# Kernel tuning notes

Hardware: AMD Instinct MI355X
Metric: run time of the kernel (lower is better)

The kernel has to match this reference:

```python
import jax, jax.numpy as jnp
import numpy as np

BN_EPS = 1e-5
W_BITS = 2
A_BITS = 2


def _quantize_k(x, k):
    # uniform quantization of x in [0,1] to k bits, straight-through estimator
    n = float(2 ** k - 1)
    q = jnp.round(x * n) / n
    return x + jax.lax.stop_gradient(q - x)


def _quant_weight(w, k):
    # DoReFa-style weight quantization to [-1, 1]
    t = jnp.tanh(w)
    t = t / (2.0 * jnp.max(jnp.abs(t))) + 0.5
    return 2.0 * _quantize_k(t, k) - 1.0


def _quant_act(x, k):
    # DoReFa-style activation quantization: clamp to [0,1], quantize
    return _quantize_k(jnp.clip(x, 0.0, 1.0), k)


def _conv3x3(x, w, stride=1):
    # x: [N,C,H,W], w: [O,I,3,3], padding=1
    return jax.lax.conv_general_dilated(
        x, w, window_strides=(stride, stride), padding=((1, 1), (1, 1)),
        dimension_numbers=('NCHW', 'OIHW', 'NCHW'))


def _bn(x, gamma, beta, mean, var):
    inv = gamma / jnp.sqrt(var + BN_EPS)           # [C]
    return x * inv[None, :, None, None] + (beta - mean * inv)[None, :, None, None]


def setup_inputs() -> dict:
    key = jax.random.key(0)
    ks = jax.random.split(key, 8)
    N, C, H, W = 64, 256, 28, 28
    x = jax.random.normal(ks[0], (N, C, H, W), dtype=jnp.float32)
    w1 = jax.random.normal(ks[1], (C, C, 3, 3), dtype=jnp.float32) * 0.05
    w2 = jax.random.normal(ks[2], (C, C, 3, 3), dtype=jnp.float32) * 0.05
    g1 = jnp.ones((C,), jnp.float32)
    b1 = jnp.zeros((C,), jnp.float32)
    m1 = jax.random.normal(ks[3], (C,), dtype=jnp.float32) * 0.1
    v1 = jax.random.uniform(ks[4], (C,), dtype=jnp.float32) + 0.5
    g2 = jnp.ones((C,), jnp.float32)
    b2 = jnp.zeros((C,), jnp.float32)
    m2 = jax.random.normal(ks[5], (C,), dtype=jnp.float32) * 0.1
    v2 = jax.random.uniform(ks[6], (C,), dtype=jnp.float32) + 0.5
    return {'x': x, 'w1': w1, 'g1': g1, 'b1': b1, 'm1': m1, 'v1': v1,
            'w2': w2, 'g2': g2, 'b2': b2, 'm2': m2, 'v2': v2}


def reference(x, w1, g1, b1, m1, v1, w2, g2, b2, m2, v2):
    residual = x
    # conv1 (2-bit quantized weights & activations) -> bn1 -> relu
    out = _conv3x3(_quant_act(x, A_BITS), _quant_weight(w1, W_BITS), stride=1)
    out = jax.nn.relu(_bn(out, g1, b1, m1, v1))
    # conv2 (2-bit quantized) -> bn2
    out = _conv3x3(_quant_act(out, A_BITS), _quant_weight(w2, W_BITS), stride=1)
    out = _bn(out, g2, b2, m2, v2)
    # residual add + relu
    return jax.nn.relu(out + residual)
```

## Files before the change

### kernel.cpp

```cpp
#include <hip/hip_runtime.h>


#define ABUF 14745600
using i32x4 = __attribute__((ext_vector_type(4))) int;

__device__ __forceinline__ void gload16(const void* g, void* l) {
  typedef const __attribute__((address_space(1))) unsigned int* gp_t;
  typedef __attribute__((address_space(3))) unsigned int* lp_t;
  __builtin_amdgcn_global_load_lds((gp_t)g, (lp_t)l, 16, 0, 0);
}

__device__ __forceinline__ int border_pix(int bp) {
  int hh, ww;
  if (bp < 30)      { hh = 0;       ww = bp; }
  else if (bp < 60) { hh = 29;      ww = bp - 30; }
  else if (bp < 88) { hh = bp - 59; ww = 0; }
  else              { hh = bp - 87; ww = 29; }
  return hh * 30 + ww;
}

__global__ void pre_k(const float* __restrict__ x, unsigned char* __restrict__ a1,
                      unsigned char* __restrict__ a2,
                      const float* __restrict__ w1, const float* __restrict__ w2,
                      float* __restrict__ partial,
                      const float* g1, const float* b1, const float* m1, const float* v1,
                      const float* g2, const float* b2, const float* m2, const float* v2,
                      float* s1, float* t1, float* s2, float* t2) {
  const int t = threadIdx.x;
  if (blockIdx.x >= 256) {
    int bx = blockIdx.x - 256;
    int ten = bx >> 6, bxl = bx & 63;
    if (ten == 0 && bxl == 0) {
      float i1 = g1[t] / sqrtf(v1[t] + 1e-5f);
      s1[t] = i1 * (1.f / 9.f);
      t1[t] = b1[t] - m1[t] * i1;
      float i2 = g2[t] / sqrtf(v2[t] + 1e-5f);
      s2[t] = i2 * (1.f / 9.f);
      t2[t] = b2[t] - m2[t] * i2;
    }
    const float4* v = (const float4*)(ten ? w2 : w1);
    float loc = 0.f;
    for (int i = bxl * 256 + t; i < 147456; i += 16384) {
      float4 f = v[i];
      loc = fmaxf(loc, fmaxf(fmaxf(fabsf(f.x), fabsf(f.y)), fmaxf(fabsf(f.z), fabsf(f.w))));
    }
    #pragma unroll
    for (int off = 32; off; off >>= 1) loc = fmaxf(loc, __shfl_xor(loc, off));
    __shared__ float red[4];
    if ((t & 63) == 0) red[t >> 6] = loc;
    __syncthreads();
    if (t == 0)
      partial[ten * 64 + bxl] = fmaxf(fmaxf(red[0], red[1]), fmaxf(red[2], red[3]));
    return;
  }
  __shared__ unsigned au[784 * 17];
  const int n = blockIdx.x >> 2, cq = blockIdx.x & 3;
  const int c4 = t >> 4, q = t & 15;

  #pragma unroll
  for (int m = 0; m < 2; ++m) {
    int s2i = t + m * 256;
    if (s2i < 464) {
      int bp = s2i >> 2, quad = s2i & 3;
      size_t off = ((size_t)n * 900 + border_pix(bp)) * 256 + cq * 64 + quad * 16;
      uint4 z = {0, 0, 0, 0};
      *(uint4*)(a1 + off) = z;
      *(uint4*)(a2 + off) = z;
    }
  }

  const float* xb = x + (size_t)n * 200704 + (cq * 64 + c4 * 4) * 784;
  #pragma unroll
  for (int k = 0; k < 13; ++k) {
    int hw4 = q + k * 16;
    if (hw4 < 196) {
      unsigned b[4][4];
      #pragma unroll
      for (int i = 0; i < 4; ++i) {
        float4 f = *(const float4*)(xb + i * 784 + hw4 * 4);
        b[i][0] = (unsigned)(int)rintf(3.f * fminf(fmaxf(f.x, 0.f), 1.f));
        b[i][1] = (unsigned)(int)rintf(3.f * fminf(fmaxf(f.y, 0.f), 1.f));
        b[i][2] = (unsigned)(int)rintf(3.f * fminf(fmaxf(f.z, 0.f), 1.f));
        b[i][3] = (unsigned)(int)rintf(3.f * fminf(fmaxf(f.w, 0.f), 1.f));
      }
      #pragma unroll
      for (int j = 0; j < 4; ++j)
        au[(hw4 * 4 + j) * 17 + c4] = b[0][j] | (b[1][j] << 8) | (b[2][j] << 16) | (b[3][j] << 24);
    }
  }
  __syncthreads();
  #pragma unroll
  for (int m = 0; m < 13; ++m) {
    int s = t + m * 256;
    if (s < 3136) {
      int pix = s >> 2, quad = s & 3;
      uint4 v;
      v.x = au[pix * 17 + quad * 4 + 0];
      v.y = au[pix * 17 + quad * 4 + 1];
      v.z = au[pix * 17 + quad * 4 + 2];
      v.w = au[pix * 17 + quad * 4 + 3];
      int hh = pix / 28, ww = pix - hh * 28;
      *(uint4*)(a1 + (((n * 30 + hh + 1) * 30) + ww + 1) * 256 + cq * 64 + quad * 16) = v;
    }
  }
}

__global__ void wquant_k(const float* __restrict__ w1, const float* __restrict__ w2,
                         const float* __restrict__ partial,
                         signed char* __restrict__ wq1, signed char* __restrict__ wq2) {
  const int oo = blockIdx.x, ten = blockIdx.y;
  const float* w = ten ? w2 : w1;
  signed char* o = ten ? wq2 : wq1;
  __shared__ float wl[2304];
  const int t = threadIdx.x;
  float pm = partial[ten * 64 + (t & 63)];
  #pragma unroll
  for (int off = 32; off; off >>= 1) pm = fmaxf(pm, __shfl_xor(pm, off));
  const float inv = 1.f / (2.f * tanhf(pm));
  #pragma unroll
  for (int k = 0; k < 9; ++k) wl[k * 256 + t] = tanhf(w[oo * 2304 + k * 256 + t]);
  __syncthreads();
  #pragma unroll
  for (int k = 0; k < 9; ++k) {
    int j = k * 256 + t, t9 = j >> 8, ci = j & 255;
    float tt = wl[ci * 9 + t9] * inv + 0.5f;
    int q = (int)rintf(tt * 3.f);
    o[oo * 2304 + j] = (signed char)(2 * q - 3);
  }
}

#define LGKM(N) do { asm volatile("s_waitcnt lgkmcnt(" #N ")" ::: "memory"); \
  __builtin_amdgcn_sched_barrier(0); } while (0)
#define SBAR0() __builtin_amdgcn_sched_barrier(0)

template <int MODE>
__global__ __launch_bounds__(512, 2) void conv_gemm(
    const unsigned char* __restrict__ act, const signed char* __restrict__ wq,
    const float* __restrict__ sC, const float* __restrict__ tC,
    const float* __restrict__ xres, unsigned char* __restrict__ actout,
    float* __restrict__ fout) {
  extern __shared__ __align__(16) char lds[];
  const int tid = threadIdx.x, wv = tid >> 6, lane = tid & 63;
  const int bswz = blockIdx.x & 7, bloc = blockIdx.x >> 3;
  const int wg = (bswz < 4 ? bswz * 25 : 100 + (bswz - 4) * 24) + bloc;
  const int pixBase = wg * 256;
  const int wvm = wv >> 2, wvn = wv & 3;
  constexpr int RAoff = (MODE == 0) ? 0 : 32768;
  constexpr int RBoff = 32768 - RAoff;

  int pixB[2][2], wB[2][2];
  {
    int s = (lane & 7) ^ ((lane >> 3) & 7);
    #pragma unroll
    for (int h = 0; h < 2; ++h)
      #pragma unroll
      for (int c = 0; c < 2; ++c) {
        int r = h * 128 + c * 64 + wv * 8 + (lane >> 3);
        int p = pixBase + r;
        int n = p / 784, rem = p % 784, hh = rem / 28, ww = rem % 28;
        pixB[h][c] = (((n * 30 + hh) * 30 + ww) << 8) + (s << 4);
        wB[h][c] = r * 2304 + (s << 4);
      }
  }
  auto tof = [](int kt) {
    int tap = kt >> 1;
    return ((tap / 3) * 30 + (tap % 3)) * 256 + ((kt & 1) << 7);
  };
  auto stagePix = [&](int h, int kt) {
    const int base = (kt & 1) * 65536 + h * 16384 + wv * 1024;
    const int toff = tof(kt);
    gload16(act + pixB[h][0] + toff, &lds[base]);
    gload16(act + pixB[h][1] + toff, &lds[base + 8192]);
  };
  auto stageW = [&](int h, int kt) {
    const int base = (kt & 1) * 65536 + 32768 + h * 16384 + wv * 1024;
    gload16(wq + wB[h][0] + kt * 128, &lds[base]);
    gload16(wq + wB[h][1] + kt * 128, &lds[base + 8192]);
  };
  auto stageT = [&](int kt) {
    if (MODE == 0) { stagePix(0, kt); stagePix(1, kt); stageW(0, kt); stageW(1, kt); }
    else           { stageW(0, kt); stageW(1, kt); stagePix(0, kt); stagePix(1, kt); }
  };

  i32x4 acc[8][4];
  #pragma unroll
  for (int i = 0; i < 8; ++i)
    #pragma unroll
    for (int j = 0; j < 4; ++j) acc[i][j] = (i32x4){0, 0, 0, 0};
  i32x4 pa[4][2], pb0[2][2], pb1[2][2];

  auto rdA = [&](int buf, int mh) {
    #pragma unroll
    for (int f = 0; f < 4; ++f) {
      int r = wvm * 128 + mh * 64 + f * 16 + (lane & 15);
      int rb = buf * 65536 + RAoff + r * 128;
      #pragma unroll
      for (int kc = 0; kc < 2; ++kc) {
        int sl = kc * 4 + (lane >> 4);
        pa[f][kc] = *(const i32x4*)&lds[rb + ((sl ^ (r & 7)) << 4)];
      }
    }
  };
  auto rdB = [&](int buf, int nh, i32x4 (*pb)[2]) {
    #pragma unroll
    for (int g = 0; g < 2; ++g) {
      int r = wvn * 64 + nh * 32 + g * 16 + (lane & 15);
      int rb = buf * 65536 + RBoff + r * 128;
      #pragma unroll
      for (int kc = 0; kc < 2; ++kc) {
        int sl = kc * 4 + (lane >> 4);
        pb[g][kc] = *(const i32x4*)&lds[rb + ((sl ^ (r & 7)) << 4)];
      }
    }
  };
  auto quad = [&](int mh, int nh, i32x4 (*pb)[2]) {
    #pragma unroll
    for (int kc = 0; kc < 2; ++kc)
      #pragma unroll
      for (int f = 0; f < 4; ++f)
        #pragma unroll
        for (int g = 0; g < 2; ++g)
          acc[mh * 4 + f][nh * 2 + g] = __builtin_amdgcn_mfma_i32_16x16x64_i8(
              pa[f][kc], pb[g][kc], acc[mh * 4 + f][nh * 2 + g], 0, 0, 0);
  };

  stageT(0); stageT(1);
  asm volatile("s_waitcnt vmcnt(8)" ::: "memory");
  SBAR0();
  __builtin_amdgcn_s_barrier();
  asm volatile("" ::: "memory");

  for (int t = 0; t < 18; ++t) {
    const int buf = t & 1;
    rdA(buf, 0); rdB(buf, 0, pb0);
    SBAR0();
    rdB(buf, 1, pb1);
    LGKM(4);
    __builtin_amdgcn_s_setprio(1); quad(0, 0, pb0); __builtin_amdgcn_s_setprio(0);
    LGKM(0);
    __builtin_amdgcn_s_setprio(1); quad(0, 1, pb1); __builtin_amdgcn_s_setprio(0);
    rdA(buf, 1);
    if (t < 17) {
      asm volatile("s_waitcnt vmcnt(0) lgkmcnt(0)" ::: "memory");
      SBAR0();
      __builtin_amdgcn_s_barrier();
      asm volatile("" ::: "memory");
      if (t < 16) stageT(t + 2);
    } else {
      LGKM(0);
    }
    __builtin_amdgcn_s_setprio(1);
    quad(1, 0, pb0); quad(1, 1, pb1);
    __builtin_amdgcn_s_setprio(0);
  }

  if (MODE == 0) {
    float sj[4], tj[4];
    #pragma unroll
    for (int j = 0; j < 4; ++j) {
      int c = wvn * 64 + j * 16 + (lane & 15);
      sj[j] = sC[c]; tj[j] = tC[c];
    }
    __syncthreads();
    #pragma unroll
    for (int i = 0; i < 8; ++i) {
      int lp0 = wvm * 128 + i * 16 + ((lane >> 4) << 2);
      #pragma unroll
      for (int j = 0; j < 4; ++j) {
        int lch = wvn * 64 + j * 16 + (lane & 15);
        #pragma unroll
        for (int r = 0; r < 4; ++r) {
          float y = (float)acc[i][j][r] * sj[j] + tj[j];
          y = fminf(fmaxf(y, 0.f), 1.f);
          int lp = lp0 + r;
          lds[lp * 256 + (lch ^ ((lp & 7) << 4))] = (char)(int)rintf(y * 3.f);
        }
      }
    }
    __syncthreads();
    int rr = tid >> 1, hf = tid & 1;
    int p = pixBase + rr;
    int n = p / 784, rem = p % 784, hh = rem / 28, ww = rem % 28;
    unsigned char* dst = actout + (((n * 30 + hh + 1) * 30 + (ww + 1)) << 8) + hf * 128;
    #pragma unroll
    for (int k = 0; k < 8; ++k) {
      uint4 v = *(const uint4*)&lds[rr * 256 + ((hf * 128 + k * 16) ^ ((rr & 7) << 4))];
      *(uint4*)(dst + k * 16) = v;
    }
  } else {
    #pragma unroll
    for (int i = 0; i < 8; ++i) {
      int c = wvm * 128 + i * 16 + ((lane >> 4) << 2) + (lane & 3);
      float sc = sC[c], tc = tC[c];
      #pragma unroll
      for (int j = 0; j < 4; ++j) {
        int a0 = acc[i][j][0], a1 = acc[i][j][1], a2 = acc[i][j][2], a3 = acc[i][j][3];
        int t0 = __builtin_amdgcn_mov_dpp(a0, 0xB1, 0xF, 0xF, true);
        int t1 = __builtin_amdgcn_mov_dpp(a1, 0xB1, 0xF, 0xF, true);
        int t2 = __builtin_amdgcn_mov_dpp(a2, 0xB1, 0xF, 0xF, true);
        int t3 = __builtin_amdgcn_mov_dpp(a3, 0xB1, 0xF, 0xF, true);
        const bool o1 = (lane & 1) != 0;
        int v0 = o1 ? t1 : a0;
        int v1 = o1 ? a1 : t0;
        int v2 = o1 ? t3 : a2;
        int v3 = o1 ? a3 : t2;
        int u0 = __builtin_amdgcn_mov_dpp(v2, 0x4E, 0xF, 0xF, true);
        int u1 = __builtin_amdgcn_mov_dpp(v3, 0x4E, 0xF, 0xF, true);
        int u2 = __builtin_amdgcn_mov_dpp(v0, 0x4E, 0xF, 0xF, true);
        int u3 = __builtin_amdgcn_mov_dpp(v1, 0x4E, 0xF, 0xF, true);
        const bool o2 = (lane & 2) != 0;
        int z0 = o2 ? u0 : v0;
        int z1 = o2 ? u1 : v1;
        int z2 = o2 ? v2 : u2;
        int z3 = o2 ? v3 : u3;
        int P = pixBase + wvn * 64 + j * 16 + (lane & 12);
        int n = P / 784, rem = P - n * 784;
        size_t addr = (size_t)n * 200704 + (size_t)c * 784 + rem;
        float4 xr = *(const float4*)(xres + addr);
        float4 y;
        y.x = fmaxf((float)z0 * sc + tc + xr.x, 0.f);
        y.y = fmaxf((float)z1 * sc + tc + xr.y, 0.f);
        y.z = fmaxf((float)z2 * sc + tc + xr.z, 0.f);
        y.w = fmaxf((float)z3 * sc + tc + xr.w, 0.f);
        *(float4*)(fout + addr) = y;
      }
    }
  }
}

extern "C" void kernel_launch(void* const* d_in, const int* in_sizes, int n_in,
                              void* d_out, int out_size, void* d_ws, size_t ws_size,
                              hipStream_t stream) {
  const float* x  = (const float*)d_in[0];
  const float* w1 = (const float*)d_in[1];
  const float* g1 = (const float*)d_in[2];
  const float* b1 = (const float*)d_in[3];
  const float* m1 = (const float*)d_in[4];
  const float* v1 = (const float*)d_in[5];
  const float* w2 = (const float*)d_in[6];
  const float* g2 = (const float*)d_in[7];
  const float* b2 = (const float*)d_in[8];
  const float* m2 = (const float*)d_in[9];
  const float* v2 = (const float*)d_in[10];

  char* ws = (char*)d_ws;
  float* partial = (float*)ws;
  float* s1 = (float*)(ws + 1024);
  float* t1 = (float*)(ws + 2048);
  float* s2 = (float*)(ws + 3072);
  float* t2 = (float*)(ws + 4096);
  unsigned char* a1 = (unsigned char*)(ws + 8192);
  unsigned char* a2 = a1 + ABUF;
  signed char* wq1 = (signed char*)(a2 + ABUF);
  signed char* wq2 = wq1 + 589824;

  void (*k0)(const unsigned char*, const signed char*, const float*, const float*,
             const float*, unsigned char*, float*) = conv_gemm<0>;
  void (*k1)(const unsigned char*, const signed char*, const float*, const float*,
             const float*, unsigned char*, float*) = conv_gemm<1>;
  hipFuncSetAttribute((const void*)k0, hipFuncAttributeMaxDynamicSharedMemorySize, 131072);
  hipFuncSetAttribute((const void*)k1, hipFuncAttributeMaxDynamicSharedMemorySize, 131072);

  pre_k<<<384, 256, 0, stream>>>(x, a1, a2, w1, w2, partial,
                                 g1, b1, m1, v1, g2, b2, m2, v2, s1, t1, s2, t2);
  wquant_k<<<dim3(256, 2), 256, 0, stream>>>(w1, w2, partial, wq1, wq2);
  conv_gemm<0><<<196, 512, 131072, stream>>>(a1, wq1, s1, t1, nullptr, a2, nullptr);
  conv_gemm<1><<<196, 512, 131072, stream>>>(a2, wq2, s2, t2, x, nullptr, (float*)d_out);
}
```

Before: 198.1 us.

## Stream B operand straight from global in MFMA layout, halve LDS staging

Weights for conv1 and the conv1 output activations are now written in a transposed, 16-byte-sliced layout, so each lane can load its B-operand fragments directly from global/L2 into registers instead of staging them through LDS. Only the A operand is double-buffered in LDS, which halves dynamic shared memory to 64KB. The main loop is reordered so the two wave groups issue their MFMA halves at different points relative to the barrier, to overlap work. In exchange, every wave re-reads B from global memory each k-step with no reuse across waves, adds a full vmcnt(0) wait per iteration, and scatters the conv1 output with strided stores.

New measurement: 206.3 us. 1.04x slower.

```diff
diff --git a/kernel.cpp b/kernel.cpp
--- a/kernel.cpp
+++ b/kernel.cpp
@@ -20,7 +20,7 @@
 }
 
 __global__ void pre_k(const float* __restrict__ x, unsigned char* __restrict__ a1,
-                      unsigned char* __restrict__ a2,
+                      unsigned char* __restrict__ a2T,
                       const float* __restrict__ w1, const float* __restrict__ w2,
                       float* __restrict__ partial,
                       const float* g1, const float* b1, const float* m1, const float* v1,
@@ -62,10 +62,17 @@
     int s2i = t + m * 256;
     if (s2i < 464) {
       int bp = s2i >> 2, quad = s2i & 3;
-      size_t off = ((size_t)n * 900 + border_pix(bp)) * 256 + cq * 64 + quad * 16;
       uint4 z = {0, 0, 0, 0};
-      *(uint4*)(a1 + off) = z;
-      *(uint4*)(a2 + off) = z;
+      *(uint4*)(a1 + ((size_t)n * 900 + border_pix(bp)) * 256 + cq * 64 + quad * 16) = z;
+    }
+  }
+  #pragma unroll
+  for (int m = 0; m < 2; ++m) {
+    int s2i = t + m * 256;
+    if (s2i < 464) {
+      int bp = s2i >> 2, sl = cq * 4 + (s2i & 3);
+      uint4 z = {0, 0, 0, 0};
+      *(uint4*)(a2T + ((size_t)sl * 57600 + n * 900 + border_pix(bp)) * 16) = z;
     }
   }
 
@@ -107,10 +114,9 @@
 
 __global__ void wquant_k(const float* __restrict__ w1, const float* __restrict__ w2,
                          const float* __restrict__ partial,
-                         signed char* __restrict__ wq1, signed char* __restrict__ wq2) {
+                         unsigned char* __restrict__ wqT1, unsigned char* __restrict__ wq2) {
   const int oo = blockIdx.x, ten = blockIdx.y;
   const float* w = ten ? w2 : w1;
-  signed char* o = ten ? wq2 : wq1;
   __shared__ float wl[2304];
   const int t = threadIdx.x;
   float pm = partial[ten * 64 + (t & 63)];
@@ -125,17 +131,23 @@
     int j = k * 256 + t, t9 = j >> 8, ci = j & 255;
     float tt = wl[ci * 9 + t9] * inv + 0.5f;
     int q = (int)rintf(tt * 3.f);
-    o[oo * 2304 + j] = (signed char)(2 * q - 3);
-  }
-}
-
-#define LGKM(N) do { asm volatile("s_waitcnt lgkmcnt(" #N ")" ::: "memory"); \
+    unsigned char val = (unsigned char)(signed char)(2 * q - 3);
+    if (ten == 0)
+      wqT1[(t9 * 16 + (ci >> 4)) * 4096 + oo * 16 + (ci & 15)] = val;
+    else
+      wq2[oo * 2304 + j] = val;
+  }
+}
+
+#define LGKM0() do { asm volatile("s_waitcnt lgkmcnt(0)" ::: "memory"); \
   __builtin_amdgcn_sched_barrier(0); } while (0)
-#define SBAR0() __builtin_amdgcn_sched_barrier(0)
+#define SP1() __builtin_amdgcn_s_setprio(1)
+#define SP0() __builtin_amdgcn_s_setprio(0)
 
 template <int MODE>
 __global__ __launch_bounds__(512, 2) void conv_gemm(
-    const unsigned char* __restrict__ act, const signed char* __restrict__ wq,
+    const unsigned char* __restrict__ actA,
+    const unsigned char* __restrict__ bsrc,
     const float* __restrict__ sC, const float* __restrict__ tC,
     const float* __restrict__ xres, unsigned char* __restrict__ actout,
     float* __restrict__ fout) {
@@ -145,10 +157,9 @@
   const int wg = (bswz < 4 ? bswz * 25 : 100 + (bswz - 4) * 24) + bloc;
   const int pixBase = wg * 256;
   const int wvm = wv >> 2, wvn = wv & 3;
-  constexpr int RAoff = (MODE == 0) ? 0 : 32768;
-  constexpr int RBoff = 32768 - RAoff;
-
-  int pixB[2][2], wB[2][2];
+  const bool grpB = (wvm == 1);
+
+  int aB[2][2];
   {
     int s = (lane & 7) ^ ((lane >> 3) & 7);
     #pragma unroll
@@ -156,30 +167,56 @@
       #pragma unroll
       for (int c = 0; c < 2; ++c) {
         int r = h * 128 + c * 64 + wv * 8 + (lane >> 3);
-        int p = pixBase + r;
-        int n = p / 784, rem = p % 784, hh = rem / 28, ww = rem % 28;
-        pixB[h][c] = (((n * 30 + hh) * 30 + ww) << 8) + (s << 4);
-        wB[h][c] = r * 2304 + (s << 4);
-      }
-  }
-  auto tof = [](int kt) {
+        if (MODE == 0) {
+          int p = pixBase + r;
+          int n = p / 784, rem = p % 784, hh = rem / 28, ww = rem % 28;
+          aB[h][c] = (((n * 30 + hh) * 30 + ww) << 8) + (s << 4);
+        } else {
+          aB[h][c] = r * 2304 + (s << 4);
+        }
+      }
+  }
+  auto tofA = [](int kt) {
     int tap = kt >> 1;
     return ((tap / 3) * 30 + (tap % 3)) * 256 + ((kt & 1) << 7);
   };
-  auto stagePix = [&](int h, int kt) {
-    const int base = (kt & 1) * 65536 + h * 16384 + wv * 1024;
-    const int toff = tof(kt);
-    gload16(act + pixB[h][0] + toff, &lds[base]);
-    gload16(act + pixB[h][1] + toff, &lds[base + 8192]);
-  };
-  auto stageW = [&](int h, int kt) {
-    const int base = (kt & 1) * 65536 + 32768 + h * 16384 + wv * 1024;
-    gload16(wq + wB[h][0] + kt * 128, &lds[base]);
-    gload16(wq + wB[h][1] + kt * 128, &lds[base + 8192]);
-  };
-  auto stageT = [&](int kt) {
-    if (MODE == 0) { stagePix(0, kt); stagePix(1, kt); stageW(0, kt); stageW(1, kt); }
-    else           { stageW(0, kt); stageW(1, kt); stagePix(0, kt); stagePix(1, kt); }
+  auto stageA = [&](int kt) {
+    const int koff = (MODE == 0) ? tofA(kt) : kt * 128;
+    #pragma unroll
+    for (int h = 0; h < 2; ++h) {
+      const int base = (kt & 1) * 32768 + h * 16384 + wv * 1024;
+      gload16(actA + aB[h][0] + koff, &lds[base]);
+      gload16(actA + aB[h][1] + koff, &lds[base + 8192]);
+    }
+  };
+
+  int bB[4];
+  #pragma unroll
+  for (int q = 0; q < 4; ++q) {
+    if (MODE == 0) {
+      int ch = wvn * 64 + q * 16 + (lane & 15);
+      bB[q] = ch * 16 + (lane >> 4) * 4096;
+    } else {
+      int p = pixBase + wvn * 64 + q * 16 + (lane & 15);
+      int n = p / 784, rem = p % 784, hh = rem / 28, ww = rem % 28;
+      bB[q] = (n * 900 + hh * 30 + ww) * 16 + (lane >> 4) * 921600;
+    }
+  }
+  i32x4 bc[4][2];
+  auto loadB = [&](int kt) {
+    const int tap = kt >> 1;
+    #pragma unroll
+    for (int q = 0; q < 4; ++q)
+      #pragma unroll
+      for (int kc = 0; kc < 2; ++kc) {
+        int off;
+        if (MODE == 0)
+          off = bB[q] + kt * 32768 + kc * 16384;
+        else
+          off = bB[q] + ((kt & 1) * 8 + kc * 4) * 921600 +
+                ((tap / 3) * 30 + (tap % 3)) * 16;
+        bc[q][kc] = *(const i32x4*)(bsrc + off);
+      }
   };
 
   i32x4 acc[8][4];
@@ -187,13 +224,13 @@
   for (int i = 0; i < 8; ++i)
     #pragma unroll
     for (int j = 0; j < 4; ++j) acc[i][j] = (i32x4){0, 0, 0, 0};
-  i32x4 pa[4][2], pb0[2][2], pb1[2][2];
+  i32x4 pa[4][2];
 
   auto rdA = [&](int buf, int mh) {
     #pragma unroll
     for (int f = 0; f < 4; ++f) {
       int r = wvm * 128 + mh * 64 + f * 16 + (lane & 15);
-      int rb = buf * 65536 + RAoff + r * 128;
+      int rb = buf * 32768 + r * 128;
       #pragma unroll
       for (int kc = 0; kc < 2; ++kc) {
         int sl = kc * 4 + (lane >> 4);
@@ -201,19 +238,7 @@
       }
     }
   };
-  auto rdB = [&](int buf, int nh, i32x4 (*pb)[2]) {
-    #pragma unroll
-    for (int g = 0; g < 2; ++g) {
-      int r = wvn * 64 + nh * 32 + g * 16 + (lane & 15);
-      int rb = buf * 65536 + RBoff + r * 128;
-      #pragma unroll
-      for (int kc = 0; kc < 2; ++kc) {
-        int sl = kc * 4 + (lane >> 4);
-        pb[g][kc] = *(const i32x4*)&lds[rb + ((sl ^ (r & 7)) << 4)];
-      }
-    }
-  };
-  auto quad = [&](int mh, int nh, i32x4 (*pb)[2]) {
+  auto quad = [&](int mh, int nh) {
     #pragma unroll
     for (int kc = 0; kc < 2; ++kc)
       #pragma unroll
@@ -221,38 +246,35 @@
         #pragma unroll
         for (int g = 0; g < 2; ++g)
           acc[mh * 4 + f][nh * 2 + g] = __builtin_amdgcn_mfma_i32_16x16x64_i8(
-              pa[f][kc], pb[g][kc], acc[mh * 4 + f][nh * 2 + g], 0, 0, 0);
-  };
-
-  stageT(0); stageT(1);
-  asm volatile("s_waitcnt vmcnt(8)" ::: "memory");
-  SBAR0();
+              pa[f][kc], bc[nh * 2 + g][kc], acc[mh * 4 + f][nh * 2 + g], 0, 0, 0);
+  };
+
+  stageA(0);
+  asm volatile("s_waitcnt vmcnt(0)" ::: "memory");
+  __builtin_amdgcn_sched_barrier(0);
   __builtin_amdgcn_s_barrier();
-  asm volatile("" ::: "memory");
 
   for (int t = 0; t < 18; ++t) {
     const int buf = t & 1;
-    rdA(buf, 0); rdB(buf, 0, pb0);
-    SBAR0();
-    rdB(buf, 1, pb1);
-    LGKM(4);
-    __builtin_amdgcn_s_setprio(1); quad(0, 0, pb0); __builtin_amdgcn_s_setprio(0);
-    LGKM(0);
-    __builtin_amdgcn_s_setprio(1); quad(0, 1, pb1); __builtin_amdgcn_s_setprio(0);
+    if (t > 0) {
+      asm volatile("s_waitcnt vmcnt(0) lgkmcnt(0)" ::: "memory");
+      __builtin_amdgcn_sched_barrier(0);
+      __builtin_amdgcn_s_barrier();
+      __builtin_amdgcn_sched_barrier(0);
+    }
+    if (t <= 16) stageA(t + 1);
+    if (grpB && t > 0) {
+      SP1(); quad(1, 0); quad(1, 1); SP0();
+    }
+    loadB(t);
+    rdA(buf, 0);
+    LGKM0();
+    SP1(); quad(0, 0); quad(0, 1); SP0();
     rdA(buf, 1);
-    if (t < 17) {
-      asm volatile("s_waitcnt vmcnt(0) lgkmcnt(0)" ::: "memory");
-      SBAR0();
-      __builtin_amdgcn_s_barrier();
-      asm volatile("" ::: "memory");
-      if (t < 16) stageT(t + 2);
-    } else {
-      LGKM(0);
-    }
-    __builtin_amdgcn_s_setprio(1);
-    quad(1, 0, pb0); quad(1, 1, pb1);
-    __builtin_amdgcn_s_setprio(0);
-  }
+    LGKM0();
+    if (!grpB) { SP1(); quad(1, 0); quad(1, 1); SP0(); }
+  }
+  if (grpB) { SP1(); quad(1, 0); quad(1, 1); SP0(); }
 
   if (MODE == 0) {
     float sj[4], tj[4];
@@ -281,11 +303,11 @@
     int rr = tid >> 1, hf = tid & 1;
     int p = pixBase + rr;
     int n = p / 784, rem = p % 784, hh = rem / 28, ww = rem % 28;
-    unsigned char* dst = actout + (((n * 30 + hh + 1) * 30 + (ww + 1)) << 8) + hf * 128;
+    int pixpad = n * 900 + (hh + 1) * 30 + (ww + 1);
     #pragma unroll
     for (int k = 0; k < 8; ++k) {
       uint4 v = *(const uint4*)&lds[rr * 256 + ((hf * 128 + k * 16) ^ ((rr & 7) << 4))];
-      *(uint4*)(dst + k * 16) = v;
+      *(uint4*)(actout + (size_t)(hf * 8 + k) * 921600 + pixpad * 16) = v;
     }
   } else {
     #pragma unroll
@@ -349,21 +371,22 @@
   float* t1 = (float*)(ws + 2048);
   float* s2 = (float*)(ws + 3072);
   float* t2 = (float*)(ws + 4096);
-  unsigned char* a1 = (unsigned char*)(ws + 8192);
-  unsigned char* a2 = a1 + ABUF;
-  signed char* wq1 = (signed char*)(a2 + ABUF);
-  signed char* wq2 = wq1 + 589824;
-
-  void (*k0)(const unsigned char*, const signed char*, const float*, const float*,
+  unsigned char* a1  = (unsigned char*)(ws + 8192);
+  unsigned char* a2T = a1 + ABUF;
+  unsigned char* wqT1 = a2T + ABUF;
+  unsigned char* wq2  = wqT1 + 589824;
+
+  void (*k0)(const unsigned char*, const unsigned char*, const float*, const float*,
              const float*, unsigned char*, float*) = conv_gemm<0>;
-  void (*k1)(const unsigned char*, const signed char*, const float*, const float*,
+  void (*k1)(const unsigned char*, const unsigned char*, const float*, const float*,
              const float*, unsigned char*, float*) = conv_gemm<1>;
-  hipFuncSetAttribute((const void*)k0, hipFuncAttributeMaxDynamicSharedMemorySize, 131072);
-  hipFuncSetAttribute((const void*)k1, hipFuncAttributeMaxDynamicSharedMemorySize, 131072);
-
-  pre_k<<<384, 256, 0, stream>>>(x, a1, a2, w1, w2, partial,
+  (void)hipFuncSetAttribute((const void*)k0, hipFuncAttributeMaxDynamicSharedMemorySize, 65536);
+  (void)hipFuncSetAttribute((const void*)k1, hipFuncAttributeMaxDynamicSharedMemorySize, 65536);
+
+  pre_k<<<384, 256, 0, stream>>>(x, a1, a2T, w1, w2, partial,
                                  g1, b1, m1, v1, g2, b2, m2, v2, s1, t1, s2, t2);
-  wquant_k<<<dim3(256, 2), 256, 0, stream>>>(w1, w2, partial, wq1, wq2);
-  conv_gemm<0><<<196, 512, 131072, stream>>>(a1, wq1, s1, t1, nullptr, a2, nullptr);
-  conv_gemm<1><<<196, 512, 131072, stream>>>(a2, wq2, s2, t2, x, nullptr, (float*)d_out);
-}
+  wquant_k<<<dim3(256, 2), 256, 0, stream>>>(w1, w2, partial, wqT1, wq2);
+  conv_gemm<0><<<196, 512, 65536, stream>>>(a1, wqT1, s1, t1, nullptr, a2T, nullptr);
+  conv_gemm<1><<<196, 512, 65536, stream>>>(wq2, a2T, s2, t2,
+                                            x, nullptr, (float*)d_out);
+}
```
